# Optimization experiments

Measured on AMD Instinct MI355X. Metric: run time of the kernel, lower is better.

The kernel has to match this reference:

```python
import jax, jax.numpy as jnp
import numpy as np

CPJ = 8
HID = 256
PARENTS = [-1,0,0,0,1,2,3,4,5,6,7,8,9,9,9,12,13,14,16,17,18,19]
SPARSE_IDX = list(range(54))

def _extend(nodes, cpj, parents=None):
    nodes = list(nodes)
    if parents is not None:
        while nodes[-1] != 0:
            nodes.append(parents[nodes[-1]])
    return [j * cpj + k for j in nodes for k in range(cpj)]

DQ_IN = _extend([0,3,6,9,12,13,14,15,16,17,18,19,20,21], CPJ, PARENTS)  # 21 nodes -> 168 ch
OUT1 = _extend([9], CPJ)          # 8 ch
OUT2 = _extend([6, 9, 12], CPJ)   # 24 ch
OUT3 = _extend([0, 3, 6], CPJ)    # 24 ch
IN_DIM = len(DQ_IN) + len(SPARSE_IDX)  # 222


def _mlp_params(key, out_dim):
    k = jax.random.split(key, 6)
    s = lambda fan_in: 1.0 / np.sqrt(fan_in)
    return (
        jax.random.uniform(k[0], (IN_DIM, HID), jnp.float32, -s(IN_DIM), s(IN_DIM)),
        jax.random.uniform(k[1], (HID,), jnp.float32, -s(IN_DIM), s(IN_DIM)),
        jax.random.uniform(k[2], (HID, HID), jnp.float32, -s(HID), s(HID)),
        jax.random.uniform(k[3], (HID,), jnp.float32, -s(HID), s(HID)),
        jax.random.uniform(k[4], (HID, out_dim), jnp.float32, -s(HID), s(HID)),
        jax.random.uniform(k[5], (out_dim,), jnp.float32, -s(HID), s(HID)),
    )


def setup_inputs() -> dict:
    key = jax.random.key(0)
    ks = jax.random.split(key, 5)
    B, T = 1024, 128
    inp = {
        'sparse_input': jax.random.normal(ks[0], (B, T, 54), jnp.float32),
        'decoder_output': jax.random.normal(ks[1], (B, T, 22 * CPJ), jnp.float32),
    }
    for i, (k, od) in enumerate(zip(ks[2:5], (len(OUT1), len(OUT2), len(OUT3))), start=1):
        p = _mlp_params(k, od)
        for j, name in enumerate(('w0', 'b0', 'w1', 'b1', 'w2', 'b2')):
            inp[f'{name}_{i}'] = p[j]
    return inp


def _mlp(x, w0, b0, w1, b1, w2, b2):
    h = jax.nn.leaky_relu(x @ w0 + b0, 0.01)
    h = jax.nn.leaky_relu(h @ w1 + b1, 0.01)
    return h @ w2 + b2


def reference(sparse_input, decoder_output,
              w0_1, b0_1, w1_1, b1_1, w2_1, b2_1,
              w0_2, b0_2, w1_2, b1_2, w2_2, b2_2,
              w0_3, b0_3, w1_3, b1_3, w2_3, b2_3):
    sp = sparse_input[:, :, jnp.array(SPARSE_IDX)]
    d = decoder_output
    # pass 1
    x = jnp.concatenate((d[:, :, jnp.array(DQ_IN)], sp), axis=2)
    res1 = _mlp(x, w0_1, b0_1, w1_1, b1_1, w2_1, b2_1)
    d = d.at[:, :, jnp.array(OUT1)].set(res1)
    # pass 2
    x = jnp.concatenate((d[:, :, jnp.array(DQ_IN)], sp), axis=2)
    res2 = _mlp(x, w0_2, b0_2, w1_2, b1_2, w2_2, b2_2)
    d = d.at[:, :, jnp.array(OUT2)].set(res2)
    # pass 3
    x = jnp.concatenate((d[:, :, jnp.array(DQ_IN)], sp), axis=2)
    res3 = _mlp(x, w0_3, b0_3, w1_3, b1_3, w2_3, b2_3)
    return res3
```

## Files before the change

kernel.cpp:

```cpp
#include <hip/hip_runtime.h>

typedef __bf16 bf16x8 __attribute__((ext_vector_type(8)));
typedef __bf16 bf16x4 __attribute__((ext_vector_type(4)));
typedef float  f32x16 __attribute__((ext_vector_type(16)));

#define DDEC  176
#define DSP   54
#define HID   256
#define RPW   32
#define WPB   4
#define BM    (RPW * WPB)
#define QSZ   16384
#define W1_OFF 65536
#define W2_OFF 131072
#define MLP_WS 139264

struct Biases { const float* b1[3]; const float* b2[3]; };

__global__ __launch_bounds__(256) void prep_weights(
    const float* __restrict__ w0a, const float* __restrict__ w1a, const float* __restrict__ w2a,
    const float* __restrict__ w0b, const float* __restrict__ w1b, const float* __restrict__ w2b,
    const float* __restrict__ w0c, const float* __restrict__ w1c, const float* __restrict__ w2c,
    const float* __restrict__ b0a, const float* __restrict__ b0b, const float* __restrict__ b0c,
    __bf16* __restrict__ ws)
{
  int idx = blockIdx.x * 256 + threadIdx.x;
  if (idx >= 3 * MLP_WS) return;
  int m = idx / MLP_WS;
  int r = idx - m * MLP_WS;
  const float* w0 = (m == 0) ? w0a : (m == 1) ? w0b : w0c;
  const float* w1 = (m == 0) ? w1a : (m == 1) ? w1b : w1c;
  const float* w2 = (m == 0) ? w2a : (m == 1) ? w2b : w2c;
  const float* b0 = (m == 0) ? b0a : (m == 1) ? b0b : b0c;
  float v;
  if (r < W1_OFF) {
    int n = r >> 8, k = r & 255;
    v = (k < 222) ? w0[k * HID + n] : (k == 222 ? b0[n] : 0.0f);
  } else if (r < W2_OFF) {
    int rr = r - W1_OFF;
    int n = rr >> 8, k = rr & 255;
    v = w1[k * HID + n];
  } else {
    int rr = r - W2_OFF;
    int n = rr >> 8, k = rr & 255;
    int od = (m == 0) ? 8 : 24;
    v = (n < od) ? w2[k * od + n] : 0.0f;
  }
  ws[idx] = (__bf16)v;
}

__device__ __forceinline__ float lrelu(float v) { return v > 0.f ? v : 0.01f * v; }

__device__ __forceinline__ void gload16(const void* g, void* l) {
  __builtin_amdgcn_global_load_lds(
      (const __attribute__((address_space(1))) void*)g,
      (__attribute__((address_space(3))) void*)l, 16, 0, 0);
}

template<int ROUNDS>
__device__ __forceinline__ void stage(const __bf16* __restrict__ wsrc, __bf16* buf, int tid) {
  #pragma unroll
  for (int r = 0; r < ROUNDS; ++r) {
    const int a  = (r * 256 + tid) * 16;
    const int lc = a >> 9;
    const int un = (a & 511) ^ ((lc & 31) << 4);
    gload16(wsrc + lc * 256 + (un >> 1), (char*)buf + r * 4096 + (tid >> 6) * 1024);
  }
}

template<int NKK>
__device__ __forceinline__ void gemm2(const __bf16* buf, const bf16x8* bfr,
                                      f32x16& acc0, f32x16& acc1, int r32, int h) {
  const int sw = r32 << 4;
  #pragma unroll
  for (int kk = 0; kk < NKK; ++kk) {
    const int inner = ((kk << 5) + (h << 4)) ^ sw;
    bf16x8 a0 = *(const bf16x8*)((const char*)buf + (r32 << 9) + inner);
    bf16x8 a1 = *(const bf16x8*)((const char*)buf + ((32 + r32) << 9) + inner);
    acc0 = __builtin_amdgcn_mfma_f32_32x32x16_bf16(a0, bfr[kk], acc0, 0, 0, 0);
    acc1 = __builtin_amdgcn_mfma_f32_32x32x16_bf16(a1, bfr[kk], acc1, 0, 0, 0);
  }
}

__device__ __forceinline__ bf16x4 shfl32(bf16x4 x) {
  union { bf16x4 v; unsigned long long u; } t;
  t.v = x;
  t.u = __shfl_xor(t.u, 32, 64);
  return t.v;
}
__device__ __forceinline__ bf16x8 cat44(bf16x4 lo, bf16x4 hi) {
  return (bf16x8){lo[0], lo[1], lo[2], lo[3], hi[0], hi[1], hi[2], hi[3]};
}

struct Frag2 { bf16x8 f0, f1; };

template<bool BIAS, bool LR>
__device__ __forceinline__ Frag2 d2frags(const f32x16 acc, const float* bias, int h) {
  bf16x4 pk[4];
  #pragma unroll
  for (int t = 0; t < 4; ++t) {
    float bx = 0.f, by = 0.f, bz = 0.f, bw = 0.f;
    if (BIAS) {
      float4 bv = *(const float4*)(bias + 8 * t + 4 * h);
      bx = bv.x; by = bv.y; bz = bv.z; bw = bv.w;
    }
    float v0 = acc[4 * t] + bx, v1 = acc[4 * t + 1] + by;
    float v2 = acc[4 * t + 2] + bz, v3 = acc[4 * t + 3] + bw;
    if (LR) { v0 = lrelu(v0); v1 = lrelu(v1); v2 = lrelu(v2); v3 = lrelu(v3); }
    pk[t] = (bf16x4){(__bf16)v0, (__bf16)v1, (__bf16)v2, (__bf16)v3};
  }
  bf16x4 r1 = shfl32(h ? pk[0] : pk[1]);
  bf16x4 r2 = shfl32(h ? pk[2] : pk[3]);
  Frag2 out;
  out.f0 = h ? cat44(r1, pk[1]) : cat44(pk[0], r1);
  out.f1 = h ? cat44(r2, pk[3]) : cat44(pk[2], r2);
  return out;
}

__device__ __forceinline__ bf16x8 packf44(float4 a, float4 b) {
  return (bf16x8){(__bf16)a.x, (__bf16)a.y, (__bf16)a.z, (__bf16)a.w,
                  (__bf16)b.x, (__bf16)b.y, (__bf16)b.z, (__bf16)b.w};
}
__device__ __forceinline__ bf16x8 packf2222(float2 a, float2 b, float2 c, float2 d) {
  return (bf16x8){(__bf16)a.x, (__bf16)a.y, (__bf16)b.x, (__bf16)b.y,
                  (__bf16)c.x, (__bf16)c.y, (__bf16)d.x, (__bf16)d.y};
}

__global__ __launch_bounds__(256, 2) void trunk_fused(
    const float* __restrict__ sparse, const float* __restrict__ dec,
    const __bf16* __restrict__ ws, float* __restrict__ out, Biases bp)
{
  __shared__ __align__(16) __bf16 lds[32768];
  __bf16* const buf0 = lds;
  __bf16* const buf1 = lds + QSZ;

  const int tid  = threadIdx.x;
  const int lane = tid & 63;
  const int wid  = tid >> 6;
  const int r32  = lane & 31;
  const int h    = lane >> 5;
  const long grow = (long)blockIdx.x * BM + wid * RPW + r32;

  stage<8>(ws, buf0, tid);

  bf16x8 xb[14];
  {
    constexpr int ND[21] = {0,3,6,9,12,13,14,15,16,17,18,19,20,21,19,17,14,9,6,3,0};
    const float* drow = dec + grow * DDEC;
    const float* srow = sparse + grow * DSP;
    #pragma unroll
    for (int kf = 0; kf < 14; ++kf) {
      if (kf <= 9) {
        const int off = (h ? ND[2 * kf + 1] : ND[2 * kf]) * 8;
        const float4* p = (const float4*)(drow + off);
        xb[kf] = packf44(p[0], p[1]);
      } else if (kf == 10) {
        if (h == 0) {
          const float4* p = (const float4*)(drow + ND[20] * 8);
          xb[kf] = packf44(p[0], p[1]);
        } else {
          const float2* q = (const float2*)(srow + 0);
          xb[kf] = packf2222(q[0], q[1], q[2], q[3]);
        }
      } else if (kf <= 12) {
        const float2* q = (const float2*)(srow + (2 * kf + h - 21) * 8);
        xb[kf] = packf2222(q[0], q[1], q[2], q[3]);
      } else {
        if (h == 0) {
          const float2* q = (const float2*)(srow + 40);
          xb[kf] = packf2222(q[0], q[1], q[2], q[3]);
        } else {
          const float2* q = (const float2*)(srow + 48);
          xb[kf] = packf2222(q[0], q[1], q[2], make_float2(1.0f, 0.0f));
        }
      }
    }
  }
  __syncthreads();
  int pb = 0;

  for (int m = 0; m < 3; ++m) {
    const __bf16* W0 = ws + m * MLP_WS;
    const __bf16* W1 = W0 + W1_OFF;
    const __bf16* W2 = W0 + W2_OFF;
    const float* b1 = bp.b1[m];
    const float* b2 = bp.b2[m];

    bf16x8 hb1[16];
    f32x16 a2 = {};

    #pragma unroll
    for (int q = 0; q < 4; ++q) {
      __bf16* cur = pb ? buf1 : buf0;
      __bf16* nxt = pb ? buf0 : buf1;
      stage<8>(q < 3 ? W0 + (q + 1) * QSZ : W1, nxt, tid);
      f32x16 acc0 = {}, acc1 = {};
      gemm2<14>(cur, xb, acc0, acc1, r32, h);
      Frag2 t0 = d2frags<false, true>(acc0, nullptr, h);
      Frag2 t1 = d2frags<false, true>(acc1, nullptr, h);
      hb1[4 * q]     = t0.f0; hb1[4 * q + 1] = t0.f1;
      hb1[4 * q + 2] = t1.f0; hb1[4 * q + 3] = t1.f1;
      __syncthreads();
      pb ^= 1;
    }

    #pragma unroll
    for (int q = 0; q < 4; ++q) {
      __bf16* cur = pb ? buf1 : buf0;
      __bf16* nxt = pb ? buf0 : buf1;
      const __bf16* w2f = W2 + r32 * 256 + h * 8 + 64 * q;
      bf16x8 wa0 = *(const bf16x8*)(w2f + 0);
      bf16x8 wa1 = *(const bf16x8*)(w2f + 16);
      bf16x8 wa2 = *(const bf16x8*)(w2f + 32);
      bf16x8 wa3 = *(const bf16x8*)(w2f + 48);
      if (q < 3)      stage<8>(W1 + (q + 1) * QSZ, nxt, tid);
      else if (m < 2) stage<8>(ws + (m + 1) * MLP_WS, nxt, tid);
      f32x16 acc0 = {}, acc1 = {};
      gemm2<16>(cur, hb1, acc0, acc1, r32, h);
      Frag2 t0 = d2frags<true, true>(acc0, b1 + 64 * q, h);
      Frag2 t1 = d2frags<true, true>(acc1, b1 + 64 * q + 32, h);
      a2 = __builtin_amdgcn_mfma_f32_32x32x16_bf16(wa0, t0.f0, a2, 0, 0, 0);
      a2 = __builtin_amdgcn_mfma_f32_32x32x16_bf16(wa1, t0.f1, a2, 0, 0, 0);
      a2 = __builtin_amdgcn_mfma_f32_32x32x16_bf16(wa2, t1.f0, a2, 0, 0, 0);
      a2 = __builtin_amdgcn_mfma_f32_32x32x16_bf16(wa3, t1.f1, a2, 0, 0, 0);
      __syncthreads();
      pb ^= 1;
    }

    if (m == 2) {
      #pragma unroll
      for (int t = 0; t < 3; ++t) {
        const int c0 = 8 * t + 4 * h;
        float4 bv = *(const float4*)(b2 + c0);
        float4 o;
        o.x = a2[4 * t]     + bv.x;
        o.y = a2[4 * t + 1] + bv.y;
        o.z = a2[4 * t + 2] + bv.z;
        o.w = a2[4 * t + 3] + bv.w;
        *(float4*)(out + grow * 24 + c0) = o;
      }
    } else {
      bf16x4 pk[3];
      #pragma unroll
      for (int t = 0; t < 3; ++t) {
        const int c0 = 8 * t + 4 * h;
        float4 bv = *(const float4*)(b2 + c0);
        pk[t] = (bf16x4){(__bf16)(a2[4 * t] + bv.x),     (__bf16)(a2[4 * t + 1] + bv.y),
                         (__bf16)(a2[4 * t + 2] + bv.z), (__bf16)(a2[4 * t + 3] + bv.w)};
      }
      if (m == 0) {
        bf16x4 r = shfl32(pk[0]);
        if (h) { bf16x8 f = cat44(r, pk[0]); xb[1] = f; xb[8] = f; }
      } else {
        bf16x4 r1 = shfl32(h ? pk[0] : pk[1]);
        bf16x4 r2 = shfl32(pk[2]);
        if (h) {
          bf16x8 fJ9 = cat44(r1, pk[1]);  xb[1] = fJ9;  xb[8] = fJ9;
        } else {
          bf16x8 fJ6  = cat44(pk[0], r1); xb[1] = fJ6;  xb[9] = fJ6;
          bf16x8 fJ12 = cat44(pk[2], r2); xb[2] = fJ12;
        }
      }
    }
  }
}

extern "C" void kernel_launch(void* const* d_in, const int* in_sizes, int n_in,
                              void* d_out, int out_size, void* d_ws, size_t ws_size,
                              hipStream_t stream)
{
  const float* sparse = (const float*)d_in[0];
  const float* dec    = (const float*)d_in[1];
  Biases bp;
  const float* w0[3]; const float* w1[3]; const float* w2[3]; const float* b0[3];
  for (int m = 0; m < 3; ++m) {
    w0[m]    = (const float*)d_in[2 + m * 6 + 0];
    b0[m]    = (const float*)d_in[2 + m * 6 + 1];
    w1[m]    = (const float*)d_in[2 + m * 6 + 2];
    bp.b1[m] = (const float*)d_in[2 + m * 6 + 3];
    w2[m]    = (const float*)d_in[2 + m * 6 + 4];
    bp.b2[m] = (const float*)d_in[2 + m * 6 + 5];
  }
  __bf16* ws = (__bf16*)d_ws;
  const int nrows = in_sizes[0] / DSP;

  const int prep_total = 3 * MLP_WS;
  prep_weights<<<(prep_total + 255) / 256, 256, 0, stream>>>(
      w0[0], w1[0], w2[0], w0[1], w1[1], w2[1], w0[2], w1[2], w2[2],
      b0[0], b0[1], b0[2], ws);

  const int nblocks = nrows / BM;
  trunk_fused<<<nblocks, 256, 0, stream>>>(sparse, dec, ws, (float*)d_out, bp);
}
```

Before: 139.2 us.

## Halve weight staging chunks to cut LDS and raise occupancy to three blocks

Weight tiles staged into LDS shrink from 64 to 32 output columns per step, so the double buffer uses 32 KB instead of 64 KB. Launch bounds rise to 3 blocks per CU. Each step now runs one MFMA accumulator chain instead of two, and takes twice as many steps with twice as many barriers. The aim is more resident waves to hide latency, at the cost of less instruction-level parallelism per wave and more synchronisation overhead.

```diff
diff --git a/kernel.cpp b/kernel.cpp
--- a/kernel.cpp
+++ b/kernel.cpp
@@ -10,7 +10,7 @@
 #define RPW   32
 #define WPB   4
 #define BM    (RPW * WPB)
-#define QSZ   16384
+#define CSZ   8192
 #define W1_OFF 65536
 #define W2_OFF 131072
 #define MLP_WS 139264
@@ -57,10 +57,9 @@
       (__attribute__((address_space(3))) void*)l, 16, 0, 0);
 }
 
-template<int ROUNDS>
 __device__ __forceinline__ void stage(const __bf16* __restrict__ wsrc, __bf16* buf, int tid) {
   #pragma unroll
-  for (int r = 0; r < ROUNDS; ++r) {
+  for (int r = 0; r < 4; ++r) {
     const int a  = (r * 256 + tid) * 16;
     const int lc = a >> 9;
     const int un = (a & 511) ^ ((lc & 31) << 4);
@@ -69,16 +68,15 @@
 }
 
 template<int NKK>
-__device__ __forceinline__ void gemm2(const __bf16* buf, const bf16x8* bfr,
-                                      f32x16& acc0, f32x16& acc1, int r32, int h) {
+__device__ __forceinline__ void gemm1(const __bf16* buf, const bf16x8* bfr,
+                                      f32x16& acc, int r32, int h) {
   const int sw = r32 << 4;
+  const char* abase = (const char*)buf + (r32 << 9);
   #pragma unroll
   for (int kk = 0; kk < NKK; ++kk) {
     const int inner = ((kk << 5) + (h << 4)) ^ sw;
-    bf16x8 a0 = *(const bf16x8*)((const char*)buf + (r32 << 9) + inner);
-    bf16x8 a1 = *(const bf16x8*)((const char*)buf + ((32 + r32) << 9) + inner);
-    acc0 = __builtin_amdgcn_mfma_f32_32x32x16_bf16(a0, bfr[kk], acc0, 0, 0, 0);
-    acc1 = __builtin_amdgcn_mfma_f32_32x32x16_bf16(a1, bfr[kk], acc1, 0, 0, 0);
+    bf16x8 a0 = *(const bf16x8*)(abase + inner);
+    acc = __builtin_amdgcn_mfma_f32_32x32x16_bf16(a0, bfr[kk], acc, 0, 0, 0);
   }
 }
 
@@ -126,13 +124,13 @@
                   (__bf16)c.x, (__bf16)c.y, (__bf16)d.x, (__bf16)d.y};
 }
 
-__global__ __launch_bounds__(256, 2) void trunk_fused(
+__global__ __launch_bounds__(256, 3) void trunk_fused(
     const float* __restrict__ sparse, const float* __restrict__ dec,
     const __bf16* __restrict__ ws, float* __restrict__ out, Biases bp)
 {
-  __shared__ __align__(16) __bf16 lds[32768];
+  __shared__ __align__(16) __bf16 lds[16384];
   __bf16* const buf0 = lds;
-  __bf16* const buf1 = lds + QSZ;
+  __bf16* const buf1 = lds + CSZ;
 
   const int tid  = threadIdx.x;
   const int lane = tid & 63;
@@ -141,7 +139,7 @@
   const int h    = lane >> 5;
   const long grow = (long)blockIdx.x * BM + wid * RPW + r32;
 
-  stage<8>(ws, buf0, tid);
+  stage(ws, buf0, tid);
 
   bf16x8 xb[14];
   {
@@ -190,39 +188,33 @@
     f32x16 a2 = {};
 
     #pragma unroll
-    for (int q = 0; q < 4; ++q) {
+    for (int c = 0; c < 8; ++c) {
       __bf16* cur = pb ? buf1 : buf0;
       __bf16* nxt = pb ? buf0 : buf1;
-      stage<8>(q < 3 ? W0 + (q + 1) * QSZ : W1, nxt, tid);
-      f32x16 acc0 = {}, acc1 = {};
-      gemm2<14>(cur, xb, acc0, acc1, r32, h);
-      Frag2 t0 = d2frags<false, true>(acc0, nullptr, h);
-      Frag2 t1 = d2frags<false, true>(acc1, nullptr, h);
-      hb1[4 * q]     = t0.f0; hb1[4 * q + 1] = t0.f1;
-      hb1[4 * q + 2] = t1.f0; hb1[4 * q + 3] = t1.f1;
+      stage(c < 7 ? W0 + (c + 1) * CSZ : W1, nxt, tid);
+      f32x16 acc = {};
+      gemm1<14>(cur, xb, acc, r32, h);
+      Frag2 t = d2frags<false, true>(acc, nullptr, h);
+      hb1[2 * c]     = t.f0;
+      hb1[2 * c + 1] = t.f1;
       __syncthreads();
       pb ^= 1;
     }
 
     #pragma unroll
-    for (int q = 0; q < 4; ++q) {
+    for (int c = 0; c < 8; ++c) {
       __bf16* cur = pb ? buf1 : buf0;
       __bf16* nxt = pb ? buf0 : buf1;
-      const __bf16* w2f = W2 + r32 * 256 + h * 8 + 64 * q;
+      const __bf16* w2f = W2 + r32 * 256 + h * 8 + 32 * c;
       bf16x8 wa0 = *(const bf16x8*)(w2f + 0);
       bf16x8 wa1 = *(const bf16x8*)(w2f + 16);
-      bf16x8 wa2 = *(const bf16x8*)(w2f + 32);
-      bf16x8 wa3 = *(const bf16x8*)(w2f + 48);
-      if (q < 3)      stage<8>(W1 + (q + 1) * QSZ, nxt, tid);
-      else if (m < 2) stage<8>(ws + (m + 1) * MLP_WS, nxt, tid);
-      f32x16 acc0 = {}, acc1 = {};
-      gemm2<16>(cur, hb1, acc0, acc1, r32, h);
-      Frag2 t0 = d2frags<true, true>(acc0, b1 + 64 * q, h);
-      Frag2 t1 = d2frags<true, true>(acc1, b1 + 64 * q + 32, h);
-      a2 = __builtin_amdgcn_mfma_f32_32x32x16_bf16(wa0, t0.f0, a2, 0, 0, 0);
-      a2 = __builtin_amdgcn_mfma_f32_32x32x16_bf16(wa1, t0.f1, a2, 0, 0, 0);
-      a2 = __builtin_amdgcn_mfma_f32_32x32x16_bf16(wa2, t1.f0, a2, 0, 0, 0);
-      a2 = __builtin_amdgcn_mfma_f32_32x32x16_bf16(wa3, t1.f1, a2, 0, 0, 0);
+      if (c < 7)      stage(W1 + (c + 1) * CSZ, nxt, tid);
+      else if (m < 2) stage(ws + (m + 1) * MLP_WS, nxt, tid);
+      f32x16 acc = {};
+      gemm1<16>(cur, hb1, acc, r32, h);
+      Frag2 t = d2frags<true, true>(acc, b1 + 32 * c, h);
+      a2 = __builtin_amdgcn_mfma_f32_32x32x16_bf16(wa0, t.f0, a2, 0, 0, 0);
+      a2 = __builtin_amdgcn_mfma_f32_32x32x16_bf16(wa1, t.f1, a2, 0, 0, 0);
       __syncthreads();
       pb ^= 1;
     }
```

New measurement: 152.1 us. 1.09x slower.
